# Performance work log

Hardware: AMD Instinct MI355X
Metric: run time of the kernel (lower is better)

The kernel has to match this reference:

```python
import jax, jax.numpy as jnp
import numpy as np

EPS = 1e-5
NUM_HEADS = 8
TOP_K = 2
CAP_FACTOR = 2  # capacity = CAP_FACTOR * T * TOP_K / E


def layernorm(x, g, b):
    m = jnp.mean(x, axis=-1, keepdims=True)
    v = jnp.var(x, axis=-1, keepdims=True)
    return (x - m) * jax.lax.rsqrt(v + EPS) * g + b


def setup_inputs() -> dict:
    key = jax.random.key(0)
    ks = jax.random.split(key, 16)
    B, S, H, E, F = 2, 2048, 512, 64, 2048
    s = 0.02
    return {
        "x": jax.random.normal(ks[0], (B, S, H), jnp.float32),
        "ln1_g": jnp.ones((H,), jnp.float32),
        "ln1_b": jnp.zeros((H,), jnp.float32),
        "wq": jax.random.normal(ks[1], (H, H), jnp.float32) * s,
        "wk": jax.random.normal(ks[2], (H, H), jnp.float32) * s,
        "wv": jax.random.normal(ks[3], (H, H), jnp.float32) * s,
        "wo": jax.random.normal(ks[4], (H, H), jnp.float32) * s,
        "ln2_g": jnp.ones((H,), jnp.float32),
        "ln2_b": jnp.zeros((H,), jnp.float32),
        "wr": jax.random.normal(ks[5], (H, E), jnp.float32) * s,
        "w1": jax.random.normal(ks[6], (E, H, F), jnp.float32) * s,
        "b1": jnp.zeros((E, F), jnp.float32),
        "w2": jax.random.normal(ks[7], (E, F, H), jnp.float32) * s,
        "b2": jnp.zeros((E, H), jnp.float32),
    }


def reference(x, ln1_g, ln1_b, wq, wk, wv, wo, ln2_g, ln2_b, wr, w1, b1, w2, b2):
    B, S, H = x.shape
    NH = NUM_HEADS
    dh = H // NH

    # ---- pre-norm multi-head self-attention + residual ----
    x1 = layernorm(x, ln1_g, ln1_b)
    q = (x1 @ wq).reshape(B, S, NH, dh)
    k = (x1 @ wk).reshape(B, S, NH, dh)
    v = (x1 @ wv).reshape(B, S, NH, dh)
    scores = jnp.einsum("bqhd,bkhd->bhqk", q, k) * (dh ** -0.5)
    p = jax.nn.softmax(scores, axis=-1)
    attn_out = jnp.einsum("bhqk,bkhd->bqhd", p, v).reshape(B, S, H) @ wo
    x = x + attn_out

    # ---- pre-norm top-2 MoE + residual ----
    x2 = layernorm(x, ln2_g, ln2_b).reshape(B * S, H)  # [T, H]
    T = B * S
    E = wr.shape[1]
    C = CAP_FACTOR * (T * TOP_K // E)  # expert capacity

    probs = jax.nn.softmax(x2 @ wr, axis=-1)            # [T, E]
    gate_v, gate_i = jax.lax.top_k(probs, TOP_K)        # [T, K]
    gate_v = gate_v / jnp.sum(gate_v, axis=-1, keepdims=True)

    ef = gate_i.reshape(-1)                              # [T*K] expert per slot
    gf = gate_v.reshape(-1)                              # [T*K] gate per slot
    oh = jax.nn.one_hot(ef, E, dtype=x2.dtype)           # [T*K, E]
    # position of each slot within its expert queue
    pos = jnp.sum((jnp.cumsum(oh, axis=0) - oh) * oh, axis=1).astype(jnp.int32)
    keep = (pos < C).astype(x2.dtype)                    # drop overflow tokens
    posc = jnp.minimum(pos, C - 1)

    tok = jnp.repeat(x2, TOP_K, axis=0) * keep[:, None]  # [T*K, H]
    buf = jnp.zeros((E, C, H), x2.dtype).at[ef, posc].add(tok)  # dispatch

    h = jax.nn.gelu(jnp.einsum("ech,ehf->ecf", buf, w1) + b1[:, None, :])
    y = jnp.einsum("ecf,efh->ech", h, w2) + b2[:, None, :]

    ys = y[ef, posc] * (gf * keep)[:, None]              # combine, [T*K, H]
    moe_out = ys.reshape(T, TOP_K, H).sum(axis=1).reshape(B, S, H)
    return x + moe_out
```

## Files before the change

kernel.cpp:

```cpp
#include <hip/hip_runtime.h>
#include <hip/hip_bf16.h>
#include <math.h>

constexpr int Bc  = 2;
constexpr int Sc  = 2048;
constexpr int Hc  = 512;
constexpr int NHc = 8;
constexpr int Tc  = Bc * Sc;
constexpr int Ec  = 64;
constexpr int Fc  = 2048;
constexpr int Cap = 256;

typedef __attribute__((ext_vector_type(8))) short bf16x8;
typedef __attribute__((ext_vector_type(4))) float f32x4;

__device__ __forceinline__ unsigned short f2b(float f) {
    union { float f; unsigned u; } v; v.f = f;
    unsigned r = v.u + 0x7FFF + ((v.u >> 16) & 1);
    return (unsigned short)(r >> 16);
}

__device__ __forceinline__ unsigned cvt_pk_bf16(float lo, float hi) {
    unsigned r;
    asm volatile("v_cvt_pk_bf16_f32 %0, %1, %2" : "=v"(r) : "v"(lo), "v"(hi));
    return r;
}

__device__ __forceinline__ float gelu_f(float x) {
    float x3 = x * x * x;
    return 0.5f * x * (1.0f + tanhf(0.7978845608028654f * (x + 0.044715f * x3)));
}

template <typename TO>
__global__ __launch_bounds__(256) void ln_kernel(const float* __restrict__ x,
                                                 const float* __restrict__ g,
                                                 const float* __restrict__ b,
                                                 TO* __restrict__ o) {
    int t = blockIdx.x;
    const float* row = x + (size_t)t * Hc;
    int tid = threadIdx.x;
    float v0 = row[tid];
    float v1 = row[tid + 256];
    float s = v0 + v1, s2 = v0 * v0 + v1 * v1;
    for (int off = 32; off; off >>= 1) {
        s  += __shfl_down(s,  off);
        s2 += __shfl_down(s2, off);
    }
    __shared__ float ls[4], ls2[4];
    int wid = tid >> 6, lane = tid & 63;
    if (lane == 0) { ls[wid] = s; ls2[wid] = s2; }
    __syncthreads();
    if (tid == 0) {
        float a = 0.f, a2 = 0.f;
        for (int i = 0; i < 4; i++) { a += ls[i]; a2 += ls2[i]; }
        ls[0] = a; ls2[0] = a2;
    }
    __syncthreads();
    float mean = ls[0] * (1.0f / Hc);
    float var  = ls2[0] * (1.0f / Hc) - mean * mean;
    float r = rsqrtf(var + 1e-5f);
    float o0 = (v0 - mean) * r * g[tid]       + b[tid];
    float o1 = (v1 - mean) * r * g[tid + 256] + b[tid + 256];
    if constexpr (sizeof(TO) == 2) {
        o[(size_t)t * Hc + tid]       = (TO)f2b(o0);
        o[(size_t)t * Hc + tid + 256] = (TO)f2b(o1);
    } else {
        o[(size_t)t * Hc + tid]       = o0;
        o[(size_t)t * Hc + tid + 256] = o1;
    }
}

template <int BM, int EPI, int SWZ, typename TC>
__global__ __launch_bounds__(BM * 2) void gemm_mfma(const unsigned short* __restrict__ A,
                                                    const float* __restrict__ W,
                                                    TC* __restrict__ C,
                                                    const float* __restrict__ X,
                                                    int M, int N, int K,
                                                    long sA, long sW, long sC, long sX,
                                                    const float* __restrict__ Wb,
                                                    const float* __restrict__ Wc) {
    int bx = blockIdx.x, bz = blockIdx.z, by = blockIdx.y;
    if (SWZ) {
        int gx = gridDim.x;
        int nwg = gx * gridDim.z;
        int flat = bx + gx * bz;
        int wg = (flat & 7) * (nwg >> 3) + (flat >> 3);
        bx = wg % gx; bz = wg / gx;
    }
    A += (size_t)bz * sA;
    if (Wb) W = (bz == 0) ? W : ((bz == 1) ? Wb : Wc);
    else    W += (size_t)bz * sW;
    C += (size_t)bz * sC;
    if (X) X += (size_t)bz * sX;
    int m0 = by * BM, n0 = bx * 128;

    __shared__ unsigned short As[BM * 72];
    __shared__ unsigned short Bs[128 * 72];

    int tid = threadIdx.x;
    int wid = tid >> 6, lane = tid & 63;
    int wr = (wid >> 1) * 64, wc = (wid & 1) * 64;
    int lr = lane & 15, lg = lane >> 4;

    f32x4 acc[4][4];
    #pragma unroll
    for (int i = 0; i < 4; i++)
        #pragma unroll
        for (int j = 0; j < 4; j++) acc[i][j] = (f32x4){0.f, 0.f, 0.f, 0.f};

    for (int k0 = 0; k0 < K; k0 += 64) {
        #pragma unroll
        for (int p = 0; p < 4; p++) {
            int e = p * 16 * BM + tid * 8;
            int row = e >> 6, col = e & 63;
            *(bf16x8*)&As[row * 72 + col] =
                *(const bf16x8*)&A[(size_t)(m0 + row) * K + k0 + col];
        }
        #pragma unroll
        for (int p = 0; p < 512 / BM; p++) {
            int kp = (tid >> 5) + p * (BM / 16);
            int c  = (tid & 31) * 4;
            const float* w0 = &W[(size_t)(k0 + 2 * kp) * N + n0 + c];
            float4 a = *(const float4*)w0;
            float4 b = *(const float4*)(w0 + N);
            int qz = 8 * ((c >> 3) & 7);
            int kof = (2 * kp) ^ qz;
            *(ushort2*)&Bs[(c + 0) * 72 + kof] = (ushort2){f2b(a.x), f2b(b.x)};
            *(ushort2*)&Bs[(c + 1) * 72 + kof] = (ushort2){f2b(a.y), f2b(b.y)};
            *(ushort2*)&Bs[(c + 2) * 72 + kof] = (ushort2){f2b(a.z), f2b(b.z)};
            *(ushort2*)&Bs[(c + 3) * 72 + kof] = (ushort2){f2b(a.w), f2b(b.w)};
        }
        __syncthreads();
        #pragma unroll
        for (int kk = 0; kk < 64; kk += 32) {
            bf16x8 af[4], bfr[4];
            #pragma unroll
            for (int i = 0; i < 4; i++) {
                af[i] = *(const bf16x8*)&As[(wr + i * 16 + lr) * 72 + kk + 8 * lg];
                int nrow = wc + i * 16 + lr;
                int qq = 8 * ((nrow >> 3) & 7);
                bfr[i] = *(const bf16x8*)&Bs[nrow * 72 + ((kk + 8 * lg) ^ qq)];
            }
            #pragma unroll
            for (int i = 0; i < 4; i++)
                #pragma unroll
                for (int j = 0; j < 4; j++)
                    acc[i][j] = __builtin_amdgcn_mfma_f32_16x16x32_bf16(af[i], bfr[j], acc[i][j], 0, 0, 0);
        }
        __syncthreads();
    }

    #pragma unroll
    for (int i = 0; i < 4; i++) {
        #pragma unroll
        for (int r = 0; r < 4; r++) {
            int m = m0 + wr + i * 16 + lg * 4 + r;
            #pragma unroll
            for (int j = 0; j < 4; j++) {
                int n = n0 + wc + j * 16 + lr;
                float vv = acc[i][j][r];
                if (EPI == 1) vv += X[(size_t)m * N + n];
                if (EPI == 2) { vv += X[n]; vv = gelu_f(vv); }
                if (EPI == 3) vv += X[n];
                if constexpr (sizeof(TC) == 2) C[(size_t)m * N + n] = (TC)f2b(vv);
                else                            C[(size_t)m * N + n] = vv;
            }
        }
    }
}

__global__ __launch_bounds__(256) void attn_mfma_kernel(const unsigned short* __restrict__ q,
                                                        const unsigned short* __restrict__ k,
                                                        const unsigned short* __restrict__ v,
                                                        unsigned short* __restrict__ o) {
    constexpr int LDK = 72;
    constexpr int NT  = Sc / 64;
    __shared__ unsigned short Ks[2][64 * LDK];
    __shared__ unsigned short Vt[2][64 * LDK];
    __shared__ unsigned short Ps[64 * LDK];

    int flat = blockIdx.x;
    int wg = (flat & 7) * 64 + (flat >> 3);
    int qt = wg & 31;
    int hb = wg >> 5;
    int hh = hb & 7, b = hb >> 3;

    int q0 = qt * 64;
    int tid = threadIdx.x;
    int wid = tid >> 6, lane = tid & 63;
    int lr = lane & 15, lg = lane >> 4;

    const unsigned short* kbase = k + (size_t)(b * Sc) * Hc + hh * 64;
    const unsigned short* vbase = v + (size_t)(b * Sc) * Hc + hh * 64;

    bf16x8 qf[2];
    {
        const unsigned short* qrow = q + ((size_t)(b * Sc + q0 + wid * 16 + lr)) * Hc + hh * 64;
        qf[0] = *(const bf16x8*)&qrow[8 * lg];
        qf[1] = *(const bf16x8*)&qrow[32 + 8 * lg];
    }

    int krow = tid >> 3;
    int kcol = (tid & 7) * 8;
    int vk2  = (tid >> 4) * 2;
    int vd4  = (tid & 15) * 4;

    bf16x8 kr[2];
    ushort4 va[2], vb2[2];

    auto load_tile = [&](int kt) {
        #pragma unroll
        for (int p = 0; p < 2; p++) {
            kr[p] = *(const bf16x8*)&kbase[(size_t)(kt * 64 + p * 32 + krow) * Hc + kcol];
            const unsigned short* vp = &vbase[(size_t)(kt * 64 + p * 32 + vk2) * Hc + vd4];
            va[p]  = *(const ushort4*)vp;
            vb2[p] = *(const ushort4*)(vp + Hc);
        }
    };
    auto vswz = [](int d, int c) { return c ^ (8 * ((d >> 3) & 7)); };
    auto store_tile = [&](int bu) {
        #pragma unroll
        for (int p = 0; p < 2; p++) {
            *(bf16x8*)&Ks[bu][(p * 32 + krow) * LDK + kcol] = kr[p];
            int k2 = p * 32 + vk2;
            *(ushort2*)&Vt[bu][(vd4 + 0) * LDK + vswz(vd4 + 0, k2)] = (ushort2){va[p].x, vb2[p].x};
            *(ushort2*)&Vt[bu][(vd4 + 1) * LDK + vswz(vd4 + 1, k2)] = (ushort2){va[p].y, vb2[p].y};
            *(ushort2*)&Vt[bu][(vd4 + 2) * LDK + vswz(vd4 + 2, k2)] = (ushort2){va[p].z, vb2[p].z};
            *(ushort2*)&Vt[bu][(vd4 + 3) * LDK + vswz(vd4 + 3, k2)] = (ushort2){va[p].w, vb2[p].w};
        }
    };

    f32x4 Oacc[4];
    #pragma unroll
    for (int nb = 0; nb < 4; nb++) Oacc[nb] = (f32x4){0.f, 0.f, 0.f, 0.f};
    float mrun = -1e30f, lrun = 0.f;
    const float scale = 0.125f;

    load_tile(0);
    store_tile(0);
    __syncthreads();

    for (int kt = 0; kt < NT; kt++) {
        int cur = kt & 1;
        if (kt + 1 < NT) load_tile(kt + 1);

        f32x4 sacc[4];
        #pragma unroll
        for (int kb = 0; kb < 4; kb++) sacc[kb] = (f32x4){0.f, 0.f, 0.f, 0.f};
        __builtin_amdgcn_s_setprio(1);
        #pragma unroll
        for (int kb = 0; kb < 4; kb++) {
            #pragma unroll
            for (int s = 0; s < 2; s++) {
                bf16x8 kf = *(const bf16x8*)&Ks[cur][(kb * 16 + lr) * LDK + 32 * s + 8 * lg];
                sacc[kb] = __builtin_amdgcn_mfma_f32_16x16x32_bf16(kf, qf[s], sacc[kb], 0, 0, 0);
            }
        }
        __builtin_amdgcn_s_setprio(0);

        float z[4][4];
        float mt = -1e30f;
        #pragma unroll
        for (int kb = 0; kb < 4; kb++)
            #pragma unroll
            for (int r = 0; r < 4; r++) {
                z[kb][r] = sacc[kb][r] * scale;
                mt = fmaxf(mt, z[kb][r]);
            }
        mt = fmaxf(mt, __shfl_xor(mt, 16));
        mt = fmaxf(mt, __shfl_xor(mt, 32));
        float mnew = fmaxf(mrun, mt);
        float sc = __expf(mrun - mnew);
        float ps = 0.f;
        float pv[4][4];
        #pragma unroll
        for (int kb = 0; kb < 4; kb++)
            #pragma unroll
            for (int r = 0; r < 4; r++) {
                pv[kb][r] = __expf(z[kb][r] - mnew);
                ps += pv[kb][r];
            }
        ps += __shfl_xor(ps, 16);
        ps += __shfl_xor(ps, 32);
        lrun = lrun * sc + ps;
        mrun = mnew;

        #pragma unroll
        for (int kb = 0; kb < 4; kb++) {
            unsigned lo = cvt_pk_bf16(pv[kb][0], pv[kb][1]);
            unsigned hi = cvt_pk_bf16(pv[kb][2], pv[kb][3]);
            *(uint2*)&Ps[(wid * 16 + lr) * LDK + kb * 16 + lg * 4] = (uint2){lo, hi};
        }
        asm volatile("s_waitcnt lgkmcnt(0)" ::: "memory");
        __builtin_amdgcn_sched_barrier(0);

        float scb[4];
        #pragma unroll
        for (int r = 0; r < 4; r++) scb[r] = __shfl(sc, lg * 4 + r);

        bf16x8 pf0 = *(const bf16x8*)&Ps[(wid * 16 + lr) * LDK + 8 * lg];
        bf16x8 pf1 = *(const bf16x8*)&Ps[(wid * 16 + lr) * LDK + 32 + 8 * lg];
        __builtin_amdgcn_s_setprio(1);
        #pragma unroll
        for (int nb = 0; nb < 4; nb++) {
            f32x4 oa = Oacc[nb];
            #pragma unroll
            for (int r = 0; r < 4; r++) oa[r] *= scb[r];
            int vrow = nb * 16 + lr;
            bf16x8 vf0 = *(const bf16x8*)&Vt[cur][vrow * LDK + vswz(vrow, 8 * lg)];
            bf16x8 vf1 = *(const bf16x8*)&Vt[cur][vrow * LDK + vswz(vrow, 32 + 8 * lg)];
            oa = __builtin_amdgcn_mfma_f32_16x16x32_bf16(pf0, vf0, oa, 0, 0, 0);
            oa = __builtin_amdgcn_mfma_f32_16x16x32_bf16(pf1, vf1, oa, 0, 0, 0);
            Oacc[nb] = oa;
        }
        __builtin_amdgcn_s_setprio(0);

        if (kt + 1 < NT) store_tile(cur ^ 1);
        __syncthreads();
    }

    float linv = 1.0f / lrun;
    unsigned short* ob = o + ((size_t)(b * Sc + q0 + wid * 16)) * Hc + hh * 64;
    #pragma unroll
    for (int r = 0; r < 4; r++) {
        float invB = __shfl(linv, lg * 4 + r);
        #pragma unroll
        for (int nb = 0; nb < 4; nb++) {
            ob[(size_t)(lg * 4 + r) * Hc + nb * 16 + lr] = f2b(Oacc[nb][r] * invB);
        }
    }
}

__global__ __launch_bounds__(256) void router_top2_kernel(const float* __restrict__ x2,
                                                          const float* __restrict__ wr,
                                                          int* __restrict__ ef,
                                                          float* __restrict__ gf) {
    int t = blockIdx.x * 4 + (threadIdx.x >> 6);
    int l = threadIdx.x & 63;
    const float* xr = x2 + (size_t)t * Hc;
    float acc = 0.f;
    for (int hhh = 0; hhh < Hc; hhh++) acc += xr[hhh] * wr[hhh * Ec + l];

    float mx = acc;
    for (int off = 32; off; off >>= 1) mx = fmaxf(mx, __shfl_xor(mx, off));
    float p = expf(acc - mx);
    float sum = p;
    for (int off = 32; off; off >>= 1) sum += __shfl_xor(sum, off);
    p /= sum;

    float v1 = p; int i1 = l;
    for (int off = 32; off; off >>= 1) {
        float ov = __shfl_xor(v1, off);
        int   oi = __shfl_xor(i1, off);
        if (ov > v1 || (ov == v1 && oi < i1)) { v1 = ov; i1 = oi; }
    }
    float v2 = (l == i1) ? -INFINITY : p; int i2 = l;
    for (int off = 32; off; off >>= 1) {
        float ov = __shfl_xor(v2, off);
        int   oi = __shfl_xor(i2, off);
        if (ov > v2 || (ov == v2 && oi < i2)) { v2 = ov; i2 = oi; }
    }
    if (l == 0) {
        float inv = 1.0f / (v1 + v2);
        ef[t * 2]     = i1;
        ef[t * 2 + 1] = i2;
        gf[t * 2]     = v1 * inv;
        gf[t * 2 + 1] = v2 * inv;
    }
}

__global__ __launch_bounds__(256) void pos_kernel(const int* __restrict__ ef,
                                                  int* __restrict__ pos) {
    int e = blockIdx.x;
    __shared__ int cnts[257];
    int tid = threadIdx.x;
    int base = tid * 32;
    int c = 0;
    for (int i = 0; i < 32; i++) c += (ef[base + i] == e) ? 1 : 0;
    cnts[tid + 1] = c;
    if (tid == 0) cnts[0] = 0;
    __syncthreads();
    if (tid == 0) {
        for (int i = 1; i <= 256; i++) cnts[i] += cnts[i - 1];
    }
    __syncthreads();
    int run = cnts[tid];
    for (int i = 0; i < 32; i++) {
        if (ef[base + i] == e) pos[base + i] = run++;
    }
}

__global__ __launch_bounds__(128) void dispatch_kernel(const float* __restrict__ x2,
                                                       const int* __restrict__ ef,
                                                       const int* __restrict__ pos,
                                                       unsigned short* __restrict__ buf) {
    int s = blockIdx.x;
    int p = pos[s];
    if (p >= Cap) return;
    int e = ef[s];
    int t = s >> 1;
    float4 vv = ((const float4*)(x2 + (size_t)t * Hc))[threadIdx.x];
    ushort4 o;
    o.x = f2b(vv.x); o.y = f2b(vv.y); o.z = f2b(vv.z); o.w = f2b(vv.w);
    ((ushort4*)(buf + ((size_t)e * Cap + p) * Hc))[threadIdx.x] = o;
}

__global__ __launch_bounds__(128) void combine_kernel(const float* __restrict__ xa,
                                                      const float* __restrict__ y,
                                                      const int* __restrict__ ef,
                                                      const int* __restrict__ pos,
                                                      const float* __restrict__ gf,
                                                      float* __restrict__ out) {
    int t = blockIdx.x;
    int d = threadIdx.x;
    float4 acc = ((const float4*)(xa + (size_t)t * Hc))[d];
    #pragma unroll
    for (int kk = 0; kk < 2; kk++) {
        int s = t * 2 + kk;
        int p = pos[s];
        if (p < Cap) {
            float w = gf[s];
            float4 yv = ((const float4*)(y + ((size_t)ef[s] * Cap + p) * Hc))[d];
            acc.x += w * yv.x;
            acc.y += w * yv.y;
            acc.z += w * yv.z;
            acc.w += w * yv.w;
        }
    }
    ((float4*)(out + (size_t)t * Hc))[d] = acc;
}

extern "C" void kernel_launch(void* const* d_in, const int* in_sizes, int n_in,
                              void* d_out, int out_size, void* d_ws, size_t ws_size,
                              hipStream_t stream) {
    const float* x     = (const float*)d_in[0];
    const float* ln1_g = (const float*)d_in[1];
    const float* ln1_b = (const float*)d_in[2];
    const float* wq    = (const float*)d_in[3];
    const float* wk    = (const float*)d_in[4];
    const float* wv    = (const float*)d_in[5];
    const float* wo    = (const float*)d_in[6];
    const float* ln2_g = (const float*)d_in[7];
    const float* ln2_b = (const float*)d_in[8];
    const float* wr    = (const float*)d_in[9];
    const float* w1    = (const float*)d_in[10];
    const float* b1    = (const float*)d_in[11];
    const float* w2    = (const float*)d_in[12];
    const float* b2    = (const float*)d_in[13];
    float* out = (float*)d_out;

    const size_t TH   = (size_t)Tc * Hc;
    const size_t ECH  = (size_t)Ec * Cap * Hc;
    const size_t ECF  = (size_t)Ec * Cap * Fc;
    const size_t HF   = (size_t)Hc * Fc;

    char* wsb = (char*)d_ws;
    size_t off = 0;
    auto alloc = [&](size_t bytes) { size_t r = off; off = (off + bytes + 255) & ~(size_t)255; return r; };
    size_t x1b_off = alloc(TH * 2);
    size_t qkv_off = alloc(TH * 2 * 3);
    size_t ab_off  = alloc(TH * 2);
    size_t xa_off  = alloc(TH * 4);
    size_t x2_off  = alloc(TH * 4);
    size_t ef_off  = alloc((size_t)Tc * 2 * 4);
    size_t pos_off = alloc((size_t)Tc * 2 * 4);
    size_t gf_off  = alloc((size_t)Tc * 2 * 4);
    size_t buf_off = alloc(ECH * 2);
    size_t h_off   = alloc(ECF * 2);
    size_t y_off   = alloc(ECH * 4);
    if (ws_size < off) return;

    unsigned short* x1b  = (unsigned short*)(wsb + x1b_off);
    unsigned short* qb   = (unsigned short*)(wsb + qkv_off);
    unsigned short* kb   = qb + TH;
    unsigned short* vb   = qb + 2 * TH;
    unsigned short* ab   = (unsigned short*)(wsb + ab_off);
    float* xa  = (float*)(wsb + xa_off);
    float* x2  = (float*)(wsb + x2_off);
    int*   ef  = (int*)(wsb + ef_off);
    int*   pos = (int*)(wsb + pos_off);
    float* gf  = (float*)(wsb + gf_off);
    unsigned short* bufb = (unsigned short*)(wsb + buf_off);
    unsigned short* h    = (unsigned short*)(wsb + h_off);
    float* y = (float*)(wsb + y_off);

    dim3 blk(256);

    ln_kernel<unsigned short><<<Tc, blk, 0, stream>>>(x, ln1_g, ln1_b, x1b);

    gemm_mfma<128, 0, 0, unsigned short><<<dim3(Hc / 128, Tc / 128, 3), blk, 0, stream>>>(
        x1b, wq, qb, nullptr, Tc, Hc, Hc, 0, 0, (long)TH, 0, wk, wv);

    attn_mfma_kernel<<<dim3(512), blk, 0, stream>>>(qb, kb, vb, ab);

    gemm_mfma<128, 1, 0, float><<<dim3(Hc / 128, Tc / 128, 1), blk, 0, stream>>>(
        ab, wo, xa, x, Tc, Hc, Hc, 0, 0, 0, 0, nullptr, nullptr);

    ln_kernel<float><<<Tc, blk, 0, stream>>>(xa, ln2_g, ln2_b, x2);

    router_top2_kernel<<<Tc / 4, blk, 0, stream>>>(x2, wr, ef, gf);

    pos_kernel<<<Ec, blk, 0, stream>>>(ef, pos);

    dispatch_kernel<<<Tc * 2, dim3(128), 0, stream>>>(x2, ef, pos, bufb);

    gemm_mfma<256, 2, 1, unsigned short><<<dim3(Fc / 128, Cap / 256, Ec), dim3(512), 0, stream>>>(
        bufb, w1, h, b1, Cap, Fc, Hc,
        (long)Cap * Hc, (long)HF, (long)Cap * Fc, (long)Fc, nullptr, nullptr);

    gemm_mfma<256, 3, 1, float><<<dim3(Hc / 128, Cap / 256, Ec), dim3(512), 0, stream>>>(
        h, w2, y, b2, Cap, Hc, Fc,
        (long)Cap * Fc, (long)HF, (long)Cap * Hc, (long)Hc, nullptr, nullptr);

    combine_kernel<<<Tc, dim3(128), 0, stream>>>(xa, y, ef, pos, gf, out);
}
```

Baseline: 350.4 us.

## Keep attention P in registers via permlane swaps, defer softmax rescale, use exp2

Drops the LDS round-trip for the softmax probability tile: the packed bf16 P values are rearranged into the MFMA A-operand layout with v_permlane32/16_swap instead of being stored to and reloaded from shared memory. It folds log2(e) into the score scale so exponentials use exp2 directly. The online-softmax rescale of the output accumulator is skipped whenever the new tile max does not exceed the running max by more than a threshold. This removes an LDS store, a wait and the loads, plus most rescale multiplies, at the cost of a wave-uniform branch and a small risk of larger exponent values in the deferred path.

After: 348.3 us. Within noise of the previous version (-0.6%).

```diff
diff --git a/kernel.cpp b/kernel.cpp
--- a/kernel.cpp
+++ b/kernel.cpp
@@ -177,7 +177,6 @@
     constexpr int NT  = Sc / 64;
     __shared__ unsigned short Ks[2][64 * LDK];
     __shared__ unsigned short Vt[2][64 * LDK];
-    __shared__ unsigned short Ps[64 * LDK];
 
     int flat = blockIdx.x;
     int wg = (flat & 7) * 64 + (flat >> 3);
@@ -234,7 +233,7 @@
     #pragma unroll
     for (int nb = 0; nb < 4; nb++) Oacc[nb] = (f32x4){0.f, 0.f, 0.f, 0.f};
     float mrun = -1e30f, lrun = 0.f;
-    const float scale = 0.125f;
+    const float SCL2 = 0.125f * 1.4426950408889634f;
 
     load_tile(0);
     store_tile(0);
@@ -264,48 +263,81 @@
         for (int kb = 0; kb < 4; kb++)
             #pragma unroll
             for (int r = 0; r < 4; r++) {
-                z[kb][r] = sacc[kb][r] * scale;
+                z[kb][r] = sacc[kb][r] * SCL2;
                 mt = fmaxf(mt, z[kb][r]);
             }
         mt = fmaxf(mt, __shfl_xor(mt, 16));
         mt = fmaxf(mt, __shfl_xor(mt, 32));
-        float mnew = fmaxf(mrun, mt);
-        float sc = __expf(mrun - mnew);
+
+        bool defer = __all(mt - mrun <= 11.0f);
+        float pv[4][4];
         float ps = 0.f;
-        float pv[4][4];
-        #pragma unroll
-        for (int kb = 0; kb < 4; kb++)
-            #pragma unroll
-            for (int r = 0; r < 4; r++) {
-                pv[kb][r] = __expf(z[kb][r] - mnew);
-                ps += pv[kb][r];
+        if (defer) {
+            #pragma unroll
+            for (int kb = 0; kb < 4; kb++)
+                #pragma unroll
+                for (int r = 0; r < 4; r++) {
+                    pv[kb][r] = __builtin_amdgcn_exp2f(z[kb][r] - mrun);
+                    ps += pv[kb][r];
+                }
+            ps += __shfl_xor(ps, 16);
+            ps += __shfl_xor(ps, 32);
+            lrun += ps;
+        } else {
+            float mnew = fmaxf(mrun, mt);
+            float sc = __builtin_amdgcn_exp2f(mrun - mnew);
+            #pragma unroll
+            for (int kb = 0; kb < 4; kb++)
+                #pragma unroll
+                for (int r = 0; r < 4; r++) {
+                    pv[kb][r] = __builtin_amdgcn_exp2f(z[kb][r] - mnew);
+                    ps += pv[kb][r];
+                }
+            ps += __shfl_xor(ps, 16);
+            ps += __shfl_xor(ps, 32);
+            lrun = lrun * sc + ps;
+            mrun = mnew;
+            float scb[4];
+            #pragma unroll
+            for (int r = 0; r < 4; r++) scb[r] = __shfl(sc, lg * 4 + r);
+            #pragma unroll
+            for (int nb = 0; nb < 4; nb++)
+                #pragma unroll
+                for (int r = 0; r < 4; r++) Oacc[nb][r] *= scb[r];
+        }
+
+        unsigned d_[4][2];
+        #pragma unroll
+        for (int kb = 0; kb < 4; kb++) {
+            d_[kb][0] = cvt_pk_bf16(pv[kb][0], pv[kb][1]);
+            d_[kb][1] = cvt_pk_bf16(pv[kb][2], pv[kb][3]);
+        }
+        unsigned pfw[2][4];
+        #pragma unroll
+        for (int s = 0; s < 2; s++) {
+            #pragma unroll
+            for (int h = 0; h < 2; h++) {
+                unsigned xx = d_[2 * s][h], yy = d_[2 * s + 1][h];
+                asm volatile("v_permlane32_swap_b32 %0, %1" : "+v"(xx), "+v"(yy));
+                asm volatile("v_permlane16_swap_b32 %0, %1" : "+v"(xx), "+v"(yy));
+                pfw[s][h]     = xx;
+                pfw[s][2 + h] = yy;
             }
-        ps += __shfl_xor(ps, 16);
-        ps += __shfl_xor(ps, 32);
-        lrun = lrun * sc + ps;
-        mrun = mnew;
-
-        #pragma unroll
-        for (int kb = 0; kb < 4; kb++) {
-            unsigned lo = cvt_pk_bf16(pv[kb][0], pv[kb][1]);
-            unsigned hi = cvt_pk_bf16(pv[kb][2], pv[kb][3]);
-            *(uint2*)&Ps[(wid * 16 + lr) * LDK + kb * 16 + lg * 4] = (uint2){lo, hi};
-        }
-        asm volatile("s_waitcnt lgkmcnt(0)" ::: "memory");
-        __builtin_amdgcn_sched_barrier(0);
-
-        float scb[4];
-        #pragma unroll
-        for (int r = 0; r < 4; r++) scb[r] = __shfl(sc, lg * 4 + r);
-
-        bf16x8 pf0 = *(const bf16x8*)&Ps[(wid * 16 + lr) * LDK + 8 * lg];
-        bf16x8 pf1 = *(const bf16x8*)&Ps[(wid * 16 + lr) * LDK + 32 + 8 * lg];
+        }
+        bf16x8 pf0, pf1;
+        *(unsigned*)&((short*)&pf0)[0] = pfw[0][0];
+        *(unsigned*)&((short*)&pf0)[2] = pfw[0][1];
+        *(unsigned*)&((short*)&pf0)[4] = pfw[0][2];
+        *(unsigned*)&((short*)&pf0)[6] = pfw[0][3];
+        *(unsigned*)&((short*)&pf1)[0] = pfw[1][0];
+        *(unsigned*)&((short*)&pf1)[2] = pfw[1][1];
+        *(unsigned*)&((short*)&pf1)[4] = pfw[1][2];
+        *(unsigned*)&((short*)&pf1)[6] = pfw[1][3];
+
         __builtin_amdgcn_s_setprio(1);
         #pragma unroll
         for (int nb = 0; nb < 4; nb++) {
             f32x4 oa = Oacc[nb];
-            #pragma unroll
-            for (int r = 0; r < 4; r++) oa[r] *= scb[r];
             int vrow = nb * 16 + lr;
             bf16x8 vf0 = *(const bf16x8*)&Vt[cur][vrow * LDK + vswz(vrow, 8 * lg)];
             bf16x8 vf1 = *(const bf16x8*)&Vt[cur][vrow * LDK + vswz(vrow, 32 + 8 * lg)];
```
